# Kernel tuning notes

Hardware: AMD Instinct MI355X
Metric: run time of the kernel (lower is better)

Reference implementation:

```python
import jax, jax.numpy as jnp
import numpy as np

N_ATOMS = 524288
D = 256
B = 16384  # number of molecules (segments)
M_STEPS = 6


def setup_inputs() -> dict:
    key = jax.random.key(0)
    k1, k2, k3 = jax.random.split(key, 3)
    atom_features = jax.random.normal(k1, (N_ATOMS, D), dtype=jnp.float32)
    atom_split = jnp.sort(jax.random.randint(k2, (N_ATOMS,), 0, B, dtype=jnp.int32))
    # LSTM weights: U is (2d, 4d); bias has forget gate initialized to 1
    U = jax.random.normal(k3, (2 * D, 4 * D), dtype=jnp.float32) * (1.0 / np.sqrt(2 * D))
    b = jnp.concatenate([
        jnp.zeros((D,), jnp.float32),
        jnp.ones((D,), jnp.float32),
        jnp.zeros((D,), jnp.float32),
        jnp.zeros((D,), jnp.float32),
    ])
    return {"atom_features": atom_features, "atom_split": atom_split, "U": U, "b": b}


def _lstm_step(q_star, c, U, b):
    z = q_star @ U + b  # [B, 4d]
    i = jax.nn.sigmoid(z[:, :D])
    f = jax.nn.sigmoid(z[:, D:2 * D])
    o = jax.nn.sigmoid(z[:, 2 * D:3 * D])
    g = jnp.tanh(z[:, 3 * D:])
    c_out = f * c + i * g
    h_out = o * jnp.tanh(c_out)
    return h_out, c_out


def reference(atom_features, atom_split, U, b):
    c = jnp.zeros((B, D), jnp.float32)
    h = jnp.zeros((B, D), jnp.float32)
    q_star = None
    for _ in range(M_STEPS):
        q_expanded = h[atom_split]                     # [N, d] gather
        e = jnp.sum(atom_features * q_expanded, axis=1)  # [N]
        e_exp = jnp.exp(e)
        e_mol = jax.ops.segment_sum(e_exp, atom_split, num_segments=B)  # [B]
        a = e_exp / e_mol[atom_split]                  # segment softmax [N]
        r = jax.ops.segment_sum(a[:, None] * atom_features, atom_split, num_segments=B)  # [B, d]
        q_star = jnp.concatenate([h, r], axis=1)       # [B, 2d]
        h, c = _lstm_step(q_star, c, U, b)
    return q_star
```

## Files before the change

### kernel.cpp

```cpp
#include <hip/hip_runtime.h>
#include <hip/hip_bf16.h>
#include <math.h>

#define N_ATOMS 524288
#define DIM 256
#define NB 16384
#define M_STEPS 6

#define SEG 64
#define NTHREADS 512
#define SEGW 8
#define AST 520

typedef _Float16 f16x8 __attribute__((ext_vector_type(8)));
typedef float f32x16 __attribute__((ext_vector_type(16)));

__device__ __forceinline__ float sigmoidf_(float z) {
    return 1.0f / (1.0f + __expf(-z));
}
__device__ __forceinline__ float tanh_fast(float z) {
    return 1.0f - 2.0f / (__expf(2.0f * z) + 1.0f);
}
__device__ __forceinline__ float2 h2f2(unsigned u) {
    union { unsigned u; _Float16 h[2]; } x; x.u = u;
    float2 r; r.x = (float)x.h[0]; r.y = (float)x.h[1]; return r;
}

__global__ void bounds_kernel(const int* __restrict__ split, int* __restrict__ lb) {
    int b = blockIdx.x * blockDim.x + threadIdx.x;
    if (b > NB) return;
    int lo = 0, hi = N_ATOMS;
    while (lo < hi) {
        int mid = (lo + hi) >> 1;
        if (split[mid] < b) lo = mid + 1; else hi = mid;
    }
    lb[b] = lo;
}

__global__ __launch_bounds__(256) void uswz_kernel(const float* __restrict__ U,
                                                   _Float16* __restrict__ uh) {
    int d = blockIdx.x * 256 + threadIdx.x;
    int f = d >> 8;
    int r = d & 255;
    int jjp = r >> 6;
    int lane = r & 63;
    int nt = f >> 5, kc = f & 31;
    int n = nt * 32 + (lane & 31);
    int k = kc * 16 + (lane >> 5) * 8 + jjp * 2;
    union { unsigned u; _Float16 h[2]; } p;
    p.h[0] = (_Float16)U[(size_t)k * 1024 + n];
    p.h[1] = (_Float16)U[(size_t)(k + 1) * 1024 + n];
    *(unsigned*)(&uh[(size_t)(f * 64 + lane) * 8 + jjp * 2]) = p.u;
}

__global__ __launch_bounds__(NTHREADS, 1) void set2set_fused_kernel(
    const float* __restrict__ x,
    const int* __restrict__ lb,
    const _Float16* __restrict__ uh,
    const float* __restrict__ bias,
    _Float16* __restrict__ xh,
    float* __restrict__ out)
{
    extern __shared__ char smem[];
    _Float16 (*A)[AST]  = (_Float16(*)[AST])smem;
    float    (*Cs)[DIM] = (float(*)[DIM])(smem + SEG * AST * 2);
    int*     lbs        = (int*)(smem + SEG * AST * 2 + SEG * DIM * 4);

    const int t    = threadIdx.x;
    const int w    = t >> 6;
    const int lane = t & 63;
    const int g    = lane >> 4;
    const int q    = lane & 15;
    const int s0seg = blockIdx.x * SEG;

    if (t <= SEG) lbs[t] = lb[s0seg + t];
    for (int idx = t; idx < SEG * 64; idx += NTHREADS) {
        int row = idx >> 6, j4 = idx & 63;
        uint2 z; z.x = 0u; z.y = 0u;
        *(uint2*)(&A[row][j4 * 4]) = z;
        float4 zf = {0.f, 0.f, 0.f, 0.f};
        *(float4*)(&Cs[row][j4 * 4]) = zf;
    }
    const int col32 = lane & 31;
    const int d     = w * 32 + col32;
    const float bi  = bias[d];
    const float bf_ = bias[256 + d];
    const float bo  = bias[512 + d];
    const float bg  = bias[768 + d];
    __syncthreads();

#define XRED(v) { v += __shfl_xor(v, 16, 64); v += __shfl_xor(v, 32, 64); }

    for (int js = 0; js < SEGW; ++js) {
        const int sl = w * SEGW + js;
        const int s = lbs[sl], e = lbs[sl + 1];
        float a0x=0.f,a0y=0.f,a0z=0.f,a0w=0.f;
        float a1x=0.f,a1y=0.f,a1z=0.f,a1w=0.f;
        float a2x=0.f,a2y=0.f,a2z=0.f,a2w=0.f;
        float a3x=0.f,a3y=0.f,a3z=0.f,a3w=0.f;
        float cnt = 0.f;
        int i = s + g;
        float4 c0={0,0,0,0}, c1={0,0,0,0}, c2={0,0,0,0}, c3={0,0,0,0};
        if (i < e) {
            const float* xr = &x[(size_t)i * DIM + q * 16];
            c0 = *(const float4*)(xr + 0);  c1 = *(const float4*)(xr + 4);
            c2 = *(const float4*)(xr + 8);  c3 = *(const float4*)(xr + 12);
        }
        while (i < e) {
            const int inext = i + 4;
            const int iload = (inext < e) ? inext : i;
            const float* xr = &x[(size_t)iload * DIM + q * 16];
            const float4 n0 = *(const float4*)(xr + 0);
            const float4 n1 = *(const float4*)(xr + 4);
            const float4 n2 = *(const float4*)(xr + 8);
            const float4 n3 = *(const float4*)(xr + 12);

            union { _Float16 h[16]; uint4 v[2]; } P;
            P.h[0]=(_Float16)c0.x; P.h[1]=(_Float16)c0.y; P.h[2]=(_Float16)c0.z; P.h[3]=(_Float16)c0.w;
            P.h[4]=(_Float16)c1.x; P.h[5]=(_Float16)c1.y; P.h[6]=(_Float16)c1.z; P.h[7]=(_Float16)c1.w;
            P.h[8]=(_Float16)c2.x; P.h[9]=(_Float16)c2.y; P.h[10]=(_Float16)c2.z; P.h[11]=(_Float16)c2.w;
            P.h[12]=(_Float16)c3.x; P.h[13]=(_Float16)c3.y; P.h[14]=(_Float16)c3.z; P.h[15]=(_Float16)c3.w;
            uint4* xw = (uint4*)(&xh[(size_t)i * DIM + q * 16]);
            xw[0] = P.v[0]; xw[1] = P.v[1];

            cnt += 1.f;
            a0x += c0.x; a0y += c0.y; a0z += c0.z; a0w += c0.w;
            a1x += c1.x; a1y += c1.y; a1z += c1.z; a1w += c1.w;
            a2x += c2.x; a2y += c2.y; a2z += c2.z; a2w += c2.w;
            a3x += c3.x; a3y += c3.y; a3z += c3.z; a3w += c3.w;
            c0=n0; c1=n1; c2=n2; c3=n3;
            i = inext;
        }
        XRED(a0x) XRED(a0y) XRED(a0z) XRED(a0w)
        XRED(a1x) XRED(a1y) XRED(a1z) XRED(a1w)
        XRED(a2x) XRED(a2y) XRED(a2z) XRED(a2w)
        XRED(a3x) XRED(a3y) XRED(a3z) XRED(a3w)
        XRED(cnt)
        const float inv = (cnt > 0.f) ? (1.0f / cnt) : 0.f;
        float vx = (g==0) ? a0x : (g==1) ? a1x : (g==2) ? a2x : a3x;
        float vy = (g==0) ? a0y : (g==1) ? a1y : (g==2) ? a2y : a3y;
        float vz = (g==0) ? a0z : (g==1) ? a1z : (g==2) ? a2z : a3z;
        float vw = (g==0) ? a0w : (g==1) ? a1w : (g==2) ? a2w : a3w;
        union { _Float16 h[4]; uint2 u; } R;
        R.h[0]=(_Float16)(vx*inv); R.h[1]=(_Float16)(vy*inv);
        R.h[2]=(_Float16)(vz*inv); R.h[3]=(_Float16)(vw*inv);
        *(uint2*)(&A[sl][256 + q * 16 + g * 4]) = R.u;
    }
    __syncthreads();

    for (int m = 0; m < M_STEPS - 1; ++m) {
        f32x16 acc[8];
        #pragma unroll
        for (int et = 0; et < 8; ++et)
            #pragma unroll
            for (int qq = 0; qq < 16; ++qq) acc[et][qq] = 0.0f;

        #pragma unroll 4
        for (int kc = 0; kc < 32; ++kc) {
            const int kof = kc * 16 + (lane >> 5) * 8;
            f16x8 af0 = *(const f16x8*)(&A[(lane & 31)][kof]);
            f16x8 af1 = *(const f16x8*)(&A[32 + (lane & 31)][kof]);
            #pragma unroll
            for (int gate = 0; gate < 4; ++gate) {
                const int nt = gate * 8 + w;
                f16x8 bfr = *(const f16x8*)(&uh[(size_t)(nt * 32 + kc) * 512 + lane * 8]);
                acc[gate * 2 + 0] = __builtin_amdgcn_mfma_f32_32x32x16_f16(af0, bfr, acc[gate * 2 + 0], 0, 0, 0);
                acc[gate * 2 + 1] = __builtin_amdgcn_mfma_f32_32x32x16_f16(af1, bfr, acc[gate * 2 + 1], 0, 0, 0);
            }
        }
        __syncthreads();

        #pragma unroll
        for (int mt = 0; mt < 2; ++mt) {
            const int rb = mt * 32 + 4 * (lane >> 5);
            #pragma unroll
            for (int reg = 0; reg < 16; ++reg) {
                const int row = rb + (reg & 3) + 8 * (reg >> 2);
                const float ig = sigmoidf_(acc[0 + mt][reg] + bi);
                const float fg = sigmoidf_(acc[2 + mt][reg] + bf_);
                const float og = sigmoidf_(acc[4 + mt][reg] + bo);
                const float gg = tanh_fast(acc[6 + mt][reg] + bg);
                const float cn = fg * Cs[row][d] + ig * gg;
                Cs[row][d] = cn;
                const float hn = og * tanh_fast(cn);
                A[row][d] = (_Float16)hn;
                if (m == M_STEPS - 2)
                    out[(size_t)(s0seg + row) * 512 + d] = hn;
            }
        }
        __syncthreads();

        const bool last = (m == M_STEPS - 2);
        for (int js = 0; js < SEGW; ++js) {
            const int sl = w * SEGW + js;
            const int s = lbs[sl], e = lbs[sl + 1];

            const uint4* hr = (const uint4*)(&A[sl][q * 16]);
            const uint4 H0 = hr[0], H1 = hr[1];
            const float2 h0 = h2f2(H0.x), h1 = h2f2(H0.y), h2_ = h2f2(H0.z), h3 = h2f2(H0.w);
            const float2 h4 = h2f2(H1.x), h5 = h2f2(H1.y), h6 = h2f2(H1.z), h7 = h2f2(H1.w);
            const float4 hv0 = {h0.x, h0.y, h1.x, h1.y};
            const float4 hv1 = {h2_.x, h2_.y, h3.x, h3.y};
            const float4 hv2 = {h4.x, h4.y, h5.x, h5.y};
            const float4 hv3 = {h6.x, h6.y, h7.x, h7.y};

            float a0x=0.f,a0y=0.f,a0z=0.f,a0w=0.f;
            float a1x=0.f,a1y=0.f,a1z=0.f,a1w=0.f;
            float a2x=0.f,a2y=0.f,a2z=0.f,a2w=0.f;
            float a3x=0.f,a3y=0.f,a3z=0.f,a3w=0.f;
            float ssum = 0.f;

            int i = s + g;
            uint4 Au = {0,0,0,0}, Bu = {0,0,0,0};
            if (i < e) {
                const uint4* xr = (const uint4*)(&xh[(size_t)i * DIM + q * 16]);
                Au = xr[0]; Bu = xr[1];
            }
            while (i < e) {
                const int inext = i + 4;
                const int iload = (inext < e) ? inext : i;
                const uint4* xr = (const uint4*)(&xh[(size_t)iload * DIM + q * 16]);
                const uint4 nA = xr[0];
                const uint4 nB = xr[1];

                const float2 p0 = h2f2(Au.x), p1 = h2f2(Au.y), p2 = h2f2(Au.z), p3 = h2f2(Au.w);
                const float2 p4 = h2f2(Bu.x), p5 = h2f2(Bu.y), p6 = h2f2(Bu.z), p7 = h2f2(Bu.w);
                const float4 c0 = {p0.x, p0.y, p1.x, p1.y};
                const float4 c1 = {p2.x, p2.y, p3.x, p3.y};
                const float4 c2 = {p4.x, p4.y, p5.x, p5.y};
                const float4 c3 = {p6.x, p6.y, p7.x, p7.y};

                float d01 = c0.x*hv0.x + c0.y*hv0.y + c0.z*hv0.z + c0.w*hv0.w
                          + c1.x*hv1.x + c1.y*hv1.y + c1.z*hv1.z + c1.w*hv1.w;
                float d23 = c2.x*hv2.x + c2.y*hv2.y + c2.z*hv2.z + c2.w*hv2.w
                          + c3.x*hv3.x + c3.y*hv3.y + c3.z*hv3.z + c3.w*hv3.w;
                float dd = d01 + d23;
                dd += __shfl_xor(dd, 1, 64);
                dd += __shfl_xor(dd, 2, 64);
                dd += __shfl_xor(dd, 4, 64);
                dd += __shfl_xor(dd, 8, 64);
                const float ee = __expf(dd);
                ssum += ee;
                a0x += ee*c0.x; a0y += ee*c0.y; a0z += ee*c0.z; a0w += ee*c0.w;
                a1x += ee*c1.x; a1y += ee*c1.y; a1z += ee*c1.z; a1w += ee*c1.w;
                a2x += ee*c2.x; a2y += ee*c2.y; a2z += ee*c2.z; a2w += ee*c2.w;
                a3x += ee*c3.x; a3y += ee*c3.y; a3z += ee*c3.z; a3w += ee*c3.w;

                Au = nA; Bu = nB;
                i = inext;
            }
            XRED(a0x) XRED(a0y) XRED(a0z) XRED(a0w)
            XRED(a1x) XRED(a1y) XRED(a1z) XRED(a1w)
            XRED(a2x) XRED(a2y) XRED(a2z) XRED(a2w)
            XRED(a3x) XRED(a3y) XRED(a3z) XRED(a3w)
            XRED(ssum)
            const float inv = (ssum > 0.f) ? (1.0f / ssum) : 0.f;
            float vx = (g==0) ? a0x : (g==1) ? a1x : (g==2) ? a2x : a3x;
            float vy = (g==0) ? a0y : (g==1) ? a1y : (g==2) ? a2y : a3y;
            float vz = (g==0) ? a0z : (g==1) ? a1z : (g==2) ? a2z : a3z;
            float vw = (g==0) ? a0w : (g==1) ? a1w : (g==2) ? a2w : a3w;
            if (last) {
                float4 v; v.x = vx*inv; v.y = vy*inv; v.z = vz*inv; v.w = vw*inv;
                *(float4*)(&out[(size_t)(s0seg + sl) * 512 + 256 + q * 16 + g * 4]) = v;
            } else {
                union { _Float16 h[4]; uint2 u; } R;
                R.h[0]=(_Float16)(vx*inv); R.h[1]=(_Float16)(vy*inv);
                R.h[2]=(_Float16)(vz*inv); R.h[3]=(_Float16)(vw*inv);
                *(uint2*)(&A[sl][256 + q * 16 + g * 4]) = R.u;
            }
        }
        if (m < M_STEPS - 2) __syncthreads();
    }
#undef XRED
}

extern "C" void kernel_launch(void* const* d_in, const int* in_sizes, int n_in,
                              void* d_out, int out_size, void* d_ws, size_t ws_size,
                              hipStream_t stream) {
    const float* x     = (const float*)d_in[0];
    const int*   split = (const int*)d_in[1];
    const float* U     = (const float*)d_in[2];
    const float* bias  = (const float*)d_in[3];
    float* out = (float*)d_out;

    char* ws = (char*)d_ws;
    const size_t lb_bytes = ((size_t)(NB + 1) * sizeof(int) + 255) & ~(size_t)255;
    int*      lb = (int*)ws;
    _Float16* uh = (_Float16*)(ws + lb_bytes);
    _Float16* xh = (_Float16*)(ws + lb_bytes + (1 << 20));

    bounds_kernel<<<(NB + 1 + 255) / 256, 256, 0, stream>>>(split, lb);
    uswz_kernel<<<1024, 256, 0, stream>>>(U, uh);

    const int smem_bytes = SEG * AST * 2 + SEG * DIM * 4 + (SEG + 1) * 4;
    set2set_fused_kernel<<<NB / SEG, NTHREADS, smem_bytes, stream>>>(
        x, lb, uh, bias, xh, out);
}
```

Before: 1.244 ms.

## Double threads per block, split MFMA rows across waves, unroll attention loop by two

Result: no change. 1.250 ms (+0.5%).

```diff
diff --git a/kernel.cpp b/kernel.cpp
--- a/kernel.cpp
+++ b/kernel.cpp
@@ -8,8 +8,8 @@
 #define M_STEPS 6
 
 #define SEG 64
-#define NTHREADS 512
-#define SEGW 8
+#define NTHREADS 1024
+#define SEGW 4
 #define AST 520
 
 typedef _Float16 f16x8 __attribute__((ext_vector_type(8)));
@@ -53,7 +53,7 @@
     *(unsigned*)(&uh[(size_t)(f * 64 + lane) * 8 + jjp * 2]) = p.u;
 }
 
-__global__ __launch_bounds__(NTHREADS, 1) void set2set_fused_kernel(
+__global__ __launch_bounds__(NTHREADS) void set2set_fused_kernel(
     const float* __restrict__ x,
     const int* __restrict__ lb,
     const _Float16* __restrict__ uh,
@@ -81,8 +81,10 @@
         float4 zf = {0.f, 0.f, 0.f, 0.f};
         *(float4*)(&Cs[row][j4 * 4]) = zf;
     }
+    const int mt    = w >> 3;
+    const int wn    = w & 7;
     const int col32 = lane & 31;
-    const int d     = w * 32 + col32;
+    const int d     = wn * 32 + col32;
     const float bi  = bias[d];
     const float bf_ = bias[256 + d];
     const float bo  = bias[512 + d];
@@ -149,37 +151,33 @@
     __syncthreads();
 
     for (int m = 0; m < M_STEPS - 1; ++m) {
-        f32x16 acc[8];
+        f32x16 acc[4];
         #pragma unroll
-        for (int et = 0; et < 8; ++et)
+        for (int et = 0; et < 4; ++et)
             #pragma unroll
             for (int qq = 0; qq < 16; ++qq) acc[et][qq] = 0.0f;
 
         #pragma unroll 4
         for (int kc = 0; kc < 32; ++kc) {
             const int kof = kc * 16 + (lane >> 5) * 8;
-            f16x8 af0 = *(const f16x8*)(&A[(lane & 31)][kof]);
-            f16x8 af1 = *(const f16x8*)(&A[32 + (lane & 31)][kof]);
+            f16x8 af = *(const f16x8*)(&A[mt * 32 + (lane & 31)][kof]);
             #pragma unroll
             for (int gate = 0; gate < 4; ++gate) {
-                const int nt = gate * 8 + w;
-                f16x8 bfr = *(const f16x8*)(&uh[(size_t)(nt * 32 + kc) * 512 + lane * 8]);
-                acc[gate * 2 + 0] = __builtin_amdgcn_mfma_f32_32x32x16_f16(af0, bfr, acc[gate * 2 + 0], 0, 0, 0);
-                acc[gate * 2 + 1] = __builtin_amdgcn_mfma_f32_32x32x16_f16(af1, bfr, acc[gate * 2 + 1], 0, 0, 0);
+                f16x8 bfr = *(const f16x8*)(&uh[(size_t)((gate * 8 + wn) * 32 + kc) * 512 + lane * 8]);
+                acc[gate] = __builtin_amdgcn_mfma_f32_32x32x16_f16(af, bfr, acc[gate], 0, 0, 0);
             }
         }
         __syncthreads();
 
-        #pragma unroll
-        for (int mt = 0; mt < 2; ++mt) {
+        {
             const int rb = mt * 32 + 4 * (lane >> 5);
             #pragma unroll
             for (int reg = 0; reg < 16; ++reg) {
                 const int row = rb + (reg & 3) + 8 * (reg >> 2);
-                const float ig = sigmoidf_(acc[0 + mt][reg] + bi);
-                const float fg = sigmoidf_(acc[2 + mt][reg] + bf_);
-                const float og = sigmoidf_(acc[4 + mt][reg] + bo);
-                const float gg = tanh_fast(acc[6 + mt][reg] + bg);
+                const float ig = sigmoidf_(acc[0][reg] + bi);
+                const float fg = sigmoidf_(acc[1][reg] + bf_);
+                const float og = sigmoidf_(acc[2][reg] + bo);
+                const float gg = tanh_fast(acc[3][reg] + bg);
                 const float cn = fg * Cs[row][d] + ig * gg;
                 Cs[row][d] = cn;
                 const float hn = og * tanh_fast(cn);
@@ -211,42 +209,64 @@
             float ssum = 0.f;
 
             int i = s + g;
-            uint4 Au = {0,0,0,0}, Bu = {0,0,0,0};
+            uint4 A0={0,0,0,0}, B0={0,0,0,0}, A1={0,0,0,0}, B1={0,0,0,0};
             if (i < e) {
-                const uint4* xr = (const uint4*)(&xh[(size_t)i * DIM + q * 16]);
-                Au = xr[0]; Bu = xr[1];
+                const uint4* xr0 = (const uint4*)(&xh[(size_t)i * DIM + q * 16]);
+                A0 = xr0[0]; B0 = xr0[1];
+                const int r1 = (i + 4 < e) ? i + 4 : i;
+                const uint4* xr1 = (const uint4*)(&xh[(size_t)r1 * DIM + q * 16]);
+                A1 = xr1[0]; B1 = xr1[1];
             }
             while (i < e) {
-                const int inext = i + 4;
-                const int iload = (inext < e) ? inext : i;
-                const uint4* xr = (const uint4*)(&xh[(size_t)iload * DIM + q * 16]);
-                const uint4 nA = xr[0];
-                const uint4 nB = xr[1];
-
-                const float2 p0 = h2f2(Au.x), p1 = h2f2(Au.y), p2 = h2f2(Au.z), p3 = h2f2(Au.w);
-                const float2 p4 = h2f2(Bu.x), p5 = h2f2(Bu.y), p6 = h2f2(Bu.z), p7 = h2f2(Bu.w);
+                const int inext = i + 8;
+                const int il0 = (inext < e) ? inext : i;
+                const int il1 = (inext + 4 < e) ? inext + 4 : i;
+                const uint4* xr0 = (const uint4*)(&xh[(size_t)il0 * DIM + q * 16]);
+                const uint4 n0a = xr0[0];
+                const uint4 n0b = xr0[1];
+                const uint4* xr1 = (const uint4*)(&xh[(size_t)il1 * DIM + q * 16]);
+                const uint4 n1a = xr1[0];
+                const uint4 n1b = xr1[1];
+
+                const float2 p0 = h2f2(A0.x), p1 = h2f2(A0.y), p2 = h2f2(A0.z), p3 = h2f2(A0.w);
+                const float2 p4 = h2f2(B0.x), p5 = h2f2(B0.y), p6 = h2f2(B0.z), p7 = h2f2(B0.w);
                 const float4 c0 = {p0.x, p0.y, p1.x, p1.y};
                 const float4 c1 = {p2.x, p2.y, p3.x, p3.y};
                 const float4 c2 = {p4.x, p4.y, p5.x, p5.y};
                 const float4 c3 = {p6.x, p6.y, p7.x, p7.y};
-
-                float d01 = c0.x*hv0.x + c0.y*hv0.y + c0.z*hv0.z + c0.w*hv0.w
-                          + c1.x*hv1.x + c1.y*hv1.y + c1.z*hv1.z + c1.w*hv1.w;
-                float d23 = c2.x*hv2.x + c2.y*hv2.y + c2.z*hv2.z + c2.w*hv2.w
-                          + c3.x*hv3.x + c3.y*hv3.y + c3.z*hv3.z + c3.w*hv3.w;
-                float dd = d01 + d23;
-                dd += __shfl_xor(dd, 1, 64);
-                dd += __shfl_xor(dd, 2, 64);
-                dd += __shfl_xor(dd, 4, 64);
-                dd += __shfl_xor(dd, 8, 64);
-                const float ee = __expf(dd);
-                ssum += ee;
-                a0x += ee*c0.x; a0y += ee*c0.y; a0z += ee*c0.z; a0w += ee*c0.w;
-                a1x += ee*c1.x; a1y += ee*c1.y; a1z += ee*c1.z; a1w += ee*c1.w;
-                a2x += ee*c2.x; a2y += ee*c2.y; a2z += ee*c2.z; a2w += ee*c2.w;
-                a3x += ee*c3.x; a3y += ee*c3.y; a3z += ee*c3.z; a3w += ee*c3.w;
-
-                Au = nA; Bu = nB;
+                const float2 q0 = h2f2(A1.x), q1 = h2f2(A1.y), q2 = h2f2(A1.z), q3 = h2f2(A1.w);
+                const float2 q4 = h2f2(B1.x), q5 = h2f2(B1.y), q6 = h2f2(B1.z), q7 = h2f2(B1.w);
+                const float4 e0 = {q0.x, q0.y, q1.x, q1.y};
+                const float4 e1 = {q2.x, q2.y, q3.x, q3.y};
+                const float4 e2 = {q4.x, q4.y, q5.x, q5.y};
+                const float4 e3 = {q6.x, q6.y, q7.x, q7.y};
+
+                float dA = c0.x*hv0.x + c0.y*hv0.y + c0.z*hv0.z + c0.w*hv0.w
+                         + c1.x*hv1.x + c1.y*hv1.y + c1.z*hv1.z + c1.w*hv1.w
+                         + c2.x*hv2.x + c2.y*hv2.y + c2.z*hv2.z + c2.w*hv2.w
+                         + c3.x*hv3.x + c3.y*hv3.y + c3.z*hv3.z + c3.w*hv3.w;
+                float dB = e0.x*hv0.x + e0.y*hv0.y + e0.z*hv0.z + e0.w*hv0.w
+                         + e1.x*hv1.x + e1.y*hv1.y + e1.z*hv1.z + e1.w*hv1.w
+                         + e2.x*hv2.x + e2.y*hv2.y + e2.z*hv2.z + e2.w*hv2.w
+                         + e3.x*hv3.x + e3.y*hv3.y + e3.z*hv3.z + e3.w*hv3.w;
+                dA += __shfl_xor(dA, 1, 64);  dB += __shfl_xor(dB, 1, 64);
+                dA += __shfl_xor(dA, 2, 64);  dB += __shfl_xor(dB, 2, 64);
+                dA += __shfl_xor(dA, 4, 64);  dB += __shfl_xor(dB, 4, 64);
+                dA += __shfl_xor(dA, 8, 64);  dB += __shfl_xor(dB, 8, 64);
+
+                const float eeA = __expf(dA);
+                const float eeB = (i + 4 < e) ? __expf(dB) : 0.0f;
+                ssum += eeA + eeB;
+                a0x += eeA*c0.x + eeB*e0.x; a0y += eeA*c0.y + eeB*e0.y;
+                a0z += eeA*c0.z + eeB*e0.z; a0w += eeA*c0.w + eeB*e0.w;
+                a1x += eeA*c1.x + eeB*e1.x; a1y += eeA*c1.y + eeB*e1.y;
+                a1z += eeA*c1.z + eeB*e1.z; a1w += eeA*c1.w + eeB*e1.w;
+                a2x += eeA*c2.x + eeB*e2.x; a2y += eeA*c2.y + eeB*e2.y;
+                a2z += eeA*c2.z + eeB*e2.z; a2w += eeA*c2.w + eeB*e2.w;
+                a3x += eeA*c3.x + eeB*e3.x; a3y += eeA*c3.y + eeB*e3.y;
+                a3z += eeA*c3.z + eeB*e3.z; a3w += eeA*c3.w + eeB*e3.w;
+
+                A0 = n0a; B0 = n0b; A1 = n1a; B1 = n1b;
                 i = inext;
             }
             XRED(a0x) XRED(a0y) XRED(a0z) XRED(a0w)
```
